# Performance work log

Hardware: AMD Instinct MI355X
Metric: run time of the kernel (lower is better)

## Reference

```python
import jax, jax.numpy as jnp
import numpy as np

BS, DX, DY = 64, 512, 512


def setup_inputs() -> dict:
    key = jax.random.key(0)
    k1, k2, k3, k4, k5 = jax.random.split(key, 5)
    # ~1/3 of bins are zero -> ragged nonzero counts per sample
    hist = jax.random.randint(k1, (BS, DX, DY), 0, 3).astype(jnp.float32)
    xlo = jax.random.uniform(k2, (BS,)) * -5.0
    ylo = jax.random.uniform(k3, (BS,)) * -5.0
    x_lims = jnp.stack([xlo, xlo + 1.0 + 9.0 * jax.random.uniform(k4, (BS,))], axis=1)
    y_lims = jnp.stack([ylo, ylo + 1.0 + 9.0 * jax.random.uniform(k5, (BS,))], axis=1)
    return {"hist": hist, "x_lims": x_lims, "y_lims": y_lims}


def _grids(hist, x_lims, y_lims):
    bs, dx, dy = hist.shape
    cxw = (x_lims[:, 1] - x_lims[:, 0]) / dx  # [bs]
    cyw = (y_lims[:, 1] - y_lims[:, 0]) / dy
    cx = (jnp.linspace(0.0, 1.0, dx)[None, :] * cxw[:, None] * (dx - 1)
          + x_lims[:, 0:1] + cxw[:, None] / 2.0)  # [bs, dx]
    cy = (jnp.linspace(0.0, 1.0, dy)[None, :] * cyw[:, None] * (dy - 1)
          + y_lims[:, 0:1] + cyw[:, None] / 2.0)  # [bs, dy]
    hc = jnp.clip(hist, 0.0, 1.0)
    grid_x = cx[:, :, None] * hc  # [bs, dx, dy]
    grid_y = cy[:, None, :] * hc
    return grid_x, grid_y


def reference(hist, x_lims, y_lims):
    # as_sequence=True path. Data-dependent pad_sequence length is not
    # jit-able, so we pad to the full grid length L=dx*dy; the first lens[b]
    # entries per row match torch's ragged output, the rest are zeros
    # (torch's pad value). Stream compaction = stable argsort on the mask.
    bs, dx, dy = hist.shape
    L = dx * dy
    grid_x, grid_y = _grids(hist, x_lims, y_lims)
    mask = (hist != 0).reshape(bs, L)
    order = jnp.argsort(jnp.where(mask, 0, 1).astype(jnp.int32), axis=1, stable=True)
    pc_x = jnp.take_along_axis(grid_x.reshape(bs, L), order, axis=1)
    pc_y = jnp.take_along_axis(grid_y.reshape(bs, L), order, axis=1)
    pc_w = jnp.take_along_axis(hist.reshape(bs, L), order, axis=1)
    pc_w = jnp.where(jnp.take_along_axis(mask, order, axis=1), pc_w, 0.0)
    pc_lens = mask.sum(axis=1).astype(jnp.int32)  # [bs]
    return jnp.stack([pc_x, pc_y], axis=-1), pc_w, pc_lens
```

## Files before the change

kernel.cpp:

```cpp
#include <hip/hip_runtime.h>

#define BS 64
#define DX 512
#define DY 512
#define L (DX * DY)
#define TILE 4096
#define T_PER_S (L / TILE)
#define THREADS 256
#define EPT (TILE / THREADS)

typedef float vfloat2 __attribute__((ext_vector_type(2)));
typedef float vfloat4 __attribute__((ext_vector_type(4)));

__global__ __launch_bounds__(THREADS) void htpc_count(
    const float* __restrict__ hist, int* __restrict__ tile_count) {
  const int tile = blockIdx.x;
  const float4* h4 = (const float4*)(hist + (size_t)tile * TILE);

  int cnt = 0;
#pragma unroll
  for (int r = 0; r < EPT / 4; ++r) {
    float4 v = h4[r * THREADS + threadIdx.x];
    cnt += (v.x != 0.f) + (v.y != 0.f) + (v.z != 0.f) + (v.w != 0.f);
  }
  const int lane = threadIdx.x & 63;
  const int wv = threadIdx.x >> 6;
#pragma unroll
  for (int d = 32; d > 0; d >>= 1) cnt += __shfl_down(cnt, d);
  __shared__ int ws[THREADS / 64];
  if (lane == 0) ws[wv] = cnt;
  __syncthreads();
  if (threadIdx.x == 0) {
    int s = 0;
#pragma unroll
    for (int i = 0; i < THREADS / 64; ++i) s += ws[i];
    tile_count[tile] = s;
  }
}

__global__ __launch_bounds__(THREADS) void htpc_fused(
    const float* __restrict__ hist, const float* __restrict__ x_lims,
    const float* __restrict__ y_lims, const int* __restrict__ tile_count,
    float* __restrict__ out_pc, float* __restrict__ out_w,
    float* __restrict__ out_lens) {
  __shared__ int sidx[TILE];
  __shared__ float sw[TILE];
  __shared__ int s_off[T_PER_S + 1];
  __shared__ int wsum[THREADS / 64];

  const int tile = blockIdx.x;
  const int b = tile >> 6;
  const int t = tile & 63;
  const size_t gbase = (size_t)tile * TILE + (size_t)threadIdx.x * EPT;
  const float4* h4 = (const float4*)(hist + gbase);

  float v[EPT];
#pragma unroll
  for (int i = 0; i < EPT / 4; ++i) {
    float4 a = h4[i];
    v[i * 4 + 0] = a.x;
    v[i * 4 + 1] = a.y;
    v[i * 4 + 2] = a.z;
    v[i * 4 + 3] = a.w;
  }

  if (threadIdx.x < 64) {
    const int c = tile_count[b * T_PER_S + threadIdx.x];
    int incl = c;
#pragma unroll
    for (int d = 1; d < 64; d <<= 1) {
      int n = __shfl_up(incl, d);
      if ((int)threadIdx.x >= d) incl += n;
    }
    s_off[threadIdx.x] = incl - c;
    if (threadIdx.x == 63) s_off[T_PER_S] = incl;
  }

  int cnt = 0;
#pragma unroll
  for (int i = 0; i < EPT; ++i) cnt += (v[i] != 0.f);

  const int lane = threadIdx.x & 63;
  const int wv = threadIdx.x >> 6;
  int incl = cnt;
#pragma unroll
  for (int d = 1; d < 64; d <<= 1) {
    int n = __shfl_up(incl, d);
    if (lane >= d) incl += n;
  }
  if (lane == 63) wsum[wv] = incl;
  __syncthreads();
  int wbase = 0, total = 0;
#pragma unroll
  for (int i = 0; i < THREADS / 64; ++i) {
    int s = wsum[i];
    if (i < wv) wbase += s;
    total += s;
  }
  int r = wbase + (incl - cnt);

  const int lidx0 = (int)(gbase - (size_t)b * L);
#pragma unroll
  for (int i = 0; i < EPT; ++i) {
    if (v[i] != 0.f) {
      sidx[r] = lidx0 + i;
      sw[r] = v[i];
      ++r;
    }
  }
  __syncthreads();

  const float xlo = x_lims[b * 2], xhi = x_lims[b * 2 + 1];
  const float ylo = y_lims[b * 2], yhi = y_lims[b * 2 + 1];
  const float cxw = (xhi - xlo) / DX;
  const float cyw = (yhi - ylo) / DY;

  const int off = s_off[t];
  const int len = s_off[T_PER_S];
  vfloat2* pc2 = (vfloat2*)out_pc + (size_t)b * L;
  float* w = out_w + (size_t)b * L;

  if (t == 0 && threadIdx.x == 0) out_lens[b] = (float)len;

  for (int k = threadIdx.x; k < total; k += THREADS) {
    const int idx = sidx[k];
    const int ix = idx >> 9;
    const int iy = idx & 511;
    vfloat2 p;
    p.x = xlo + cxw * ((float)ix + 0.5f);
    p.y = ylo + cyw * ((float)iy + 0.5f);
    __builtin_nontemporal_store(p, pc2 + (off + k));
    __builtin_nontemporal_store(sw[k], w + (off + k));
  }

  const int begin = t * TILE;
  const int end = begin + TILE;
  int s0 = (len > begin) ? len : begin;
  if (s0 < end) {
    int a0 = s0;
    if (a0 & 1) {
      if (threadIdx.x == 0) {
        const vfloat2 z2 = {0.f, 0.f};
        __builtin_nontemporal_store(z2, pc2 + a0);
      }
      ++a0;
    }
    {
      vfloat4* p4 = (vfloat4*)(pc2 + a0);
      const int n4 = (end - a0) >> 1;
      const vfloat4 z4 = {0.f, 0.f, 0.f, 0.f};
      for (int k = threadIdx.x; k < n4; k += THREADS)
        __builtin_nontemporal_store(z4, p4 + k);
    }
    const int head = (s0 + 3) & ~3;
    if (threadIdx.x < (head - s0) && (s0 + (int)threadIdx.x) < end)
      __builtin_nontemporal_store(0.f, w + s0 + threadIdx.x);
    if (head < end) {
      vfloat4* w4 = (vfloat4*)(w + head);
      const int n4 = (end - head) >> 2;
      const vfloat4 z4 = {0.f, 0.f, 0.f, 0.f};
      for (int k = threadIdx.x; k < n4; k += THREADS)
        __builtin_nontemporal_store(z4, w4 + k);
    }
  }
}

extern "C" void kernel_launch(void* const* d_in, const int* in_sizes, int n_in,
                              void* d_out, int out_size, void* d_ws,
                              size_t ws_size, hipStream_t stream) {
  const float* hist = (const float*)d_in[0];
  const float* x_lims = (const float*)d_in[1];
  const float* y_lims = (const float*)d_in[2];

  float* out = (float*)d_out;
  float* out_pc = out;
  float* out_w = out + (size_t)BS * L * 2;
  float* out_lens = out_w + (size_t)BS * L;

  int* tile_count = (int*)d_ws;

  htpc_count<<<BS * T_PER_S, THREADS, 0, stream>>>(hist, tile_count);
  htpc_fused<<<BS * T_PER_S, THREADS, 0, stream>>>(
      hist, x_lims, y_lims, tile_count, out_pc, out_w, out_lens);
}
```

Before: 262.3 us.

## Merge count and scatter kernels into one cooperative kernel with grid sync

Replaces the two-kernel count-then-compact pipeline with a single cooperative kernel. Each block handles four tiles: it counts nonzeros, waits at a grid-wide barrier, then computes offsets and scatters compacted points and zero padding. The aim is to remove the second kernel launch and its gap. In exchange it adds a grid sync, fewer blocks (1024), and the second pass rereads hist for each tile. Residency needs 4 blocks per CU and about 32KB LDS per block.

After: 398.8 us. +52.1%, slower.

```diff
diff --git a/kernel.cpp b/kernel.cpp
--- a/kernel.cpp
+++ b/kernel.cpp
@@ -1,4 +1,7 @@
 #include <hip/hip_runtime.h>
+#include <hip/hip_cooperative_groups.h>
+
+namespace cg = cooperative_groups;
 
 #define BS 64
 #define DX 512
@@ -8,39 +11,16 @@
 #define T_PER_S (L / TILE)
 #define THREADS 256
 #define EPT (TILE / THREADS)
+#define TPB 4
+#define NBLK ((BS * T_PER_S) / TPB)
+#define BLK_PER_S (T_PER_S / TPB)
 
 typedef float vfloat2 __attribute__((ext_vector_type(2)));
 typedef float vfloat4 __attribute__((ext_vector_type(4)));
 
-__global__ __launch_bounds__(THREADS) void htpc_count(
-    const float* __restrict__ hist, int* __restrict__ tile_count) {
-  const int tile = blockIdx.x;
-  const float4* h4 = (const float4*)(hist + (size_t)tile * TILE);
-
-  int cnt = 0;
-#pragma unroll
-  for (int r = 0; r < EPT / 4; ++r) {
-    float4 v = h4[r * THREADS + threadIdx.x];
-    cnt += (v.x != 0.f) + (v.y != 0.f) + (v.z != 0.f) + (v.w != 0.f);
-  }
-  const int lane = threadIdx.x & 63;
-  const int wv = threadIdx.x >> 6;
-#pragma unroll
-  for (int d = 32; d > 0; d >>= 1) cnt += __shfl_down(cnt, d);
-  __shared__ int ws[THREADS / 64];
-  if (lane == 0) ws[wv] = cnt;
-  __syncthreads();
-  if (threadIdx.x == 0) {
-    int s = 0;
-#pragma unroll
-    for (int i = 0; i < THREADS / 64; ++i) s += ws[i];
-    tile_count[tile] = s;
-  }
-}
-
-__global__ __launch_bounds__(THREADS) void htpc_fused(
+__global__ __launch_bounds__(THREADS, 4) void htpc_all(
     const float* __restrict__ hist, const float* __restrict__ x_lims,
-    const float* __restrict__ y_lims, const int* __restrict__ tile_count,
+    const float* __restrict__ y_lims, int* __restrict__ tile_count,
     float* __restrict__ out_pc, float* __restrict__ out_w,
     float* __restrict__ out_lens) {
   __shared__ int sidx[TILE];
@@ -48,21 +28,32 @@
   __shared__ int s_off[T_PER_S + 1];
   __shared__ int wsum[THREADS / 64];
 
-  const int tile = blockIdx.x;
-  const int b = tile >> 6;
-  const int t = tile & 63;
-  const size_t gbase = (size_t)tile * TILE + (size_t)threadIdx.x * EPT;
-  const float4* h4 = (const float4*)(hist + gbase);
+  const int g = blockIdx.x;
+  const int b = g / BLK_PER_S;
+  const int tile0 = g * TPB;
+  const int lane = threadIdx.x & 63;
+  const int wv = threadIdx.x >> 6;
 
-  float v[EPT];
+  for (int tt = 0; tt < TPB; ++tt) {
+    const int tile = tile0 + tt;
+    const float4* h4 = (const float4*)(hist + (size_t)tile * TILE);
+    int cnt = 0;
 #pragma unroll
-  for (int i = 0; i < EPT / 4; ++i) {
-    float4 a = h4[i];
-    v[i * 4 + 0] = a.x;
-    v[i * 4 + 1] = a.y;
-    v[i * 4 + 2] = a.z;
-    v[i * 4 + 3] = a.w;
+    for (int r = 0; r < EPT / 4; ++r) {
+      float4 v = h4[r * THREADS + threadIdx.x];
+      cnt += (v.x != 0.f) + (v.y != 0.f) + (v.z != 0.f) + (v.w != 0.f);
+    }
+#pragma unroll
+    for (int d = 32; d > 0; d >>= 1) cnt += __shfl_down(cnt, d);
+    if (lane == 0) wsum[wv] = cnt;
+    __syncthreads();
+    if (threadIdx.x == 0)
+      tile_count[tile] = wsum[0] + wsum[1] + wsum[2] + wsum[3];
+    __syncthreads();
   }
+
+  __threadfence();
+  cg::this_grid().sync();
 
   if (threadIdx.x < 64) {
     const int c = tile_count[b * T_PER_S + threadIdx.x];
@@ -73,94 +64,109 @@
       if ((int)threadIdx.x >= d) incl += n;
     }
     s_off[threadIdx.x] = incl - c;
-    if (threadIdx.x == 63) s_off[T_PER_S] = incl;
-  }
-
-  int cnt = 0;
-#pragma unroll
-  for (int i = 0; i < EPT; ++i) cnt += (v[i] != 0.f);
-
-  const int lane = threadIdx.x & 63;
-  const int wv = threadIdx.x >> 6;
-  int incl = cnt;
-#pragma unroll
-  for (int d = 1; d < 64; d <<= 1) {
-    int n = __shfl_up(incl, d);
-    if (lane >= d) incl += n;
-  }
-  if (lane == 63) wsum[wv] = incl;
-  __syncthreads();
-  int wbase = 0, total = 0;
-#pragma unroll
-  for (int i = 0; i < THREADS / 64; ++i) {
-    int s = wsum[i];
-    if (i < wv) wbase += s;
-    total += s;
-  }
-  int r = wbase + (incl - cnt);
-
-  const int lidx0 = (int)(gbase - (size_t)b * L);
-#pragma unroll
-  for (int i = 0; i < EPT; ++i) {
-    if (v[i] != 0.f) {
-      sidx[r] = lidx0 + i;
-      sw[r] = v[i];
-      ++r;
+    if (threadIdx.x == 63) {
+      s_off[T_PER_S] = incl;
+      if ((g % BLK_PER_S) == 0) out_lens[b] = (float)incl;
     }
   }
-  __syncthreads();
 
   const float xlo = x_lims[b * 2], xhi = x_lims[b * 2 + 1];
   const float ylo = y_lims[b * 2], yhi = y_lims[b * 2 + 1];
   const float cxw = (xhi - xlo) / DX;
   const float cyw = (yhi - ylo) / DY;
 
-  const int off = s_off[t];
-  const int len = s_off[T_PER_S];
   vfloat2* pc2 = (vfloat2*)out_pc + (size_t)b * L;
   float* w = out_w + (size_t)b * L;
 
-  if (t == 0 && threadIdx.x == 0) out_lens[b] = (float)len;
+  for (int tt = 0; tt < TPB; ++tt) {
+    const int tile = tile0 + tt;
+    const int t = tile & (T_PER_S - 1);
+    const size_t gbase = (size_t)tile * TILE + (size_t)threadIdx.x * EPT;
+    const float4* h4 = (const float4*)(hist + gbase);
 
-  for (int k = threadIdx.x; k < total; k += THREADS) {
-    const int idx = sidx[k];
-    const int ix = idx >> 9;
-    const int iy = idx & 511;
-    vfloat2 p;
-    p.x = xlo + cxw * ((float)ix + 0.5f);
-    p.y = ylo + cyw * ((float)iy + 0.5f);
-    __builtin_nontemporal_store(p, pc2 + (off + k));
-    __builtin_nontemporal_store(sw[k], w + (off + k));
-  }
+    float v[EPT];
+#pragma unroll
+    for (int i = 0; i < EPT / 4; ++i) {
+      float4 a = h4[i];
+      v[i * 4 + 0] = a.x;
+      v[i * 4 + 1] = a.y;
+      v[i * 4 + 2] = a.z;
+      v[i * 4 + 3] = a.w;
+    }
+    int cnt = 0;
+#pragma unroll
+    for (int i = 0; i < EPT; ++i) cnt += (v[i] != 0.f);
 
-  const int begin = t * TILE;
-  const int end = begin + TILE;
-  int s0 = (len > begin) ? len : begin;
-  if (s0 < end) {
-    int a0 = s0;
-    if (a0 & 1) {
-      if (threadIdx.x == 0) {
-        const vfloat2 z2 = {0.f, 0.f};
-        __builtin_nontemporal_store(z2, pc2 + a0);
+    int incl = cnt;
+#pragma unroll
+    for (int d = 1; d < 64; d <<= 1) {
+      int n = __shfl_up(incl, d);
+      if (lane >= d) incl += n;
+    }
+    if (lane == 63) wsum[wv] = incl;
+    __syncthreads();
+    int wbase = 0, total = 0;
+#pragma unroll
+    for (int i = 0; i < THREADS / 64; ++i) {
+      int s = wsum[i];
+      if (i < wv) wbase += s;
+      total += s;
+    }
+    int r = wbase + (incl - cnt);
+
+    const int lidx0 = (int)(gbase - (size_t)b * L);
+#pragma unroll
+    for (int i = 0; i < EPT; ++i) {
+      if (v[i] != 0.f) {
+        sidx[r] = lidx0 + i;
+        sw[r] = v[i];
+        ++r;
       }
-      ++a0;
     }
-    {
-      vfloat4* p4 = (vfloat4*)(pc2 + a0);
-      const int n4 = (end - a0) >> 1;
-      const vfloat4 z4 = {0.f, 0.f, 0.f, 0.f};
-      for (int k = threadIdx.x; k < n4; k += THREADS)
-        __builtin_nontemporal_store(z4, p4 + k);
+    const int off = s_off[t];
+    const int len = s_off[T_PER_S];
+    __syncthreads();
+
+    for (int k = threadIdx.x; k < total; k += THREADS) {
+      const int idx = sidx[k];
+      const int ix = idx >> 9;
+      const int iy = idx & 511;
+      vfloat2 p;
+      p.x = xlo + cxw * ((float)ix + 0.5f);
+      p.y = ylo + cyw * ((float)iy + 0.5f);
+      __builtin_nontemporal_store(p, pc2 + (off + k));
+      __builtin_nontemporal_store(sw[k], w + (off + k));
     }
-    const int head = (s0 + 3) & ~3;
-    if (threadIdx.x < (head - s0) && (s0 + (int)threadIdx.x) < end)
-      __builtin_nontemporal_store(0.f, w + s0 + threadIdx.x);
-    if (head < end) {
-      vfloat4* w4 = (vfloat4*)(w + head);
-      const int n4 = (end - head) >> 2;
-      const vfloat4 z4 = {0.f, 0.f, 0.f, 0.f};
-      for (int k = threadIdx.x; k < n4; k += THREADS)
-        __builtin_nontemporal_store(z4, w4 + k);
+
+    const int begin = t * TILE;
+    const int end = begin + TILE;
+    int s0 = (len > begin) ? len : begin;
+    if (s0 < end) {
+      int a0 = s0;
+      if (a0 & 1) {
+        if (threadIdx.x == 0) {
+          const vfloat2 z2 = {0.f, 0.f};
+          __builtin_nontemporal_store(z2, pc2 + a0);
+        }
+        ++a0;
+      }
+      {
+        vfloat4* p4 = (vfloat4*)(pc2 + a0);
+        const int n4 = (end - a0) >> 1;
+        const vfloat4 z4 = {0.f, 0.f, 0.f, 0.f};
+        for (int k = threadIdx.x; k < n4; k += THREADS)
+          __builtin_nontemporal_store(z4, p4 + k);
+      }
+      const int head = (s0 + 3) & ~3;
+      if (threadIdx.x < (head - s0) && (s0 + (int)threadIdx.x) < end)
+        __builtin_nontemporal_store(0.f, w + s0 + threadIdx.x);
+      if (head < end) {
+        vfloat4* w4 = (vfloat4*)(w + head);
+        const int n4 = (end - head) >> 2;
+        const vfloat4 z4 = {0.f, 0.f, 0.f, 0.f};
+        for (int k = threadIdx.x; k < n4; k += THREADS)
+          __builtin_nontemporal_store(z4, w4 + k);
+      }
     }
   }
 }
@@ -179,7 +185,9 @@
 
   int* tile_count = (int*)d_ws;
 
-  htpc_count<<<BS * T_PER_S, THREADS, 0, stream>>>(hist, tile_count);
-  htpc_fused<<<BS * T_PER_S, THREADS, 0, stream>>>(
-      hist, x_lims, y_lims, tile_count, out_pc, out_w, out_lens);
+  void* args[] = {(void*)&hist, (void*)&x_lims, (void*)&y_lims,
+                  (void*)&tile_count, (void*)&out_pc, (void*)&out_w,
+                  (void*)&out_lens};
+  hipLaunchCooperativeKernel((const void*)htpc_all, dim3(NBLK), dim3(THREADS),
+                             args, 0, stream);
 }
```
